# Optimization experiments

Measured on AMD Instinct MI355X. Metric: run time of the kernel, lower is better.

Reference implementation:

```python
import jax, jax.numpy as jnp
import numpy as np

D_IN = 1024
D_OUT = 1024
NUM_HEADS = 16
HEAD_DIM = D_OUT // NUM_HEADS
WINDOW = 256


def setup_inputs() -> dict:
    key = jax.random.key(0)
    ks = jax.random.split(key, 6)
    s = 0.02
    x = jax.random.normal(ks[0], (2, 2048, D_IN), dtype=jnp.float32)
    Wq = jax.random.normal(ks[1], (D_IN, D_OUT), dtype=jnp.float32) * s
    Wk = jax.random.normal(ks[2], (D_IN, D_OUT), dtype=jnp.float32) * s
    Wv = jax.random.normal(ks[3], (D_IN, D_OUT), dtype=jnp.float32) * s
    Wo = jax.random.normal(ks[4], (D_OUT, D_OUT), dtype=jnp.float32) * s
    bo = jnp.zeros((D_OUT,), dtype=jnp.float32)
    return {"x": x, "Wq": Wq, "Wk": Wk, "Wv": Wv, "Wo": Wo, "bo": bo}


def reference(x, Wq, Wk, Wv, Wo, bo):
    b, s, _ = x.shape
    # project and split heads: [b, h, s, hd]
    def heads(t):
        return t.reshape(b, s, NUM_HEADS, HEAD_DIM).transpose(0, 2, 1, 3)
    q = heads(x @ Wq)
    k = heads(x @ Wk)
    v = heads(x @ Wv)
    scores = jnp.einsum('bhqd,bhkd->bhqk', q, k) / jnp.sqrt(jnp.float32(HEAD_DIM))
    # symmetric sliding-window band: |i - j| <= WINDOW
    i = jnp.arange(s)
    band = jnp.abs(i[:, None] - i[None, :]) <= WINDOW  # [s, s]
    scores = jnp.where(band[None, None], scores, -jnp.inf)
    probs = jax.nn.softmax(scores, axis=-1)  # dropout=0.0 -> identity
    ctx = jnp.einsum('bhqk,bhkd->bhqd', probs, v)
    ctx = ctx.transpose(0, 2, 1, 3).reshape(b, s, D_OUT)
    return ctx @ Wo + bo
```

## Files before the change

### kernel.cpp

```cpp
#include <hip/hip_runtime.h>
#include <hip/hip_bf16.h>

typedef __bf16 bf16_t;
typedef __bf16 bf16x8 __attribute__((ext_vector_type(8)));
typedef __bf16 bf16x4 __attribute__((ext_vector_type(4)));
typedef float  f32x4  __attribute__((ext_vector_type(4)));

#define SEQ    2048
#define BATCH  2
#define NHEAD  16
#define HDIM   64
#define DMODEL 1024
#define WIN    256

__device__ __forceinline__ void async_load16(const void* g, void* l) {
    __builtin_amdgcn_global_load_lds(
        (const __attribute__((address_space(1))) char*)(uintptr_t)g,
        (__attribute__((address_space(3))) char*)(uintptr_t)l, 16, 0, 0);
}

__global__ __launch_bounds__(256) void prep_kernel(
    const float* __restrict__ x, const float* __restrict__ Wq,
    const float* __restrict__ Wk, const float* __restrict__ Wv,
    const float* __restrict__ Wo, bf16_t* __restrict__ xb,
    bf16_t* __restrict__ Wt) {
    const int bid = blockIdx.x, tid = threadIdx.x;
    if (bid < 1024) {
        __shared__ float t64[64][65];
        const int mat = bid >> 8, tile = bid & 255;
        const int k0 = (tile >> 4) * 64, n0 = (tile & 15) * 64;
        const float* W = (mat == 0) ? Wq : (mat == 1) ? Wk : (mat == 2) ? Wv : Wo;
        bf16_t* out = Wt + (size_t)mat * DMODEL * DMODEL;
        const int r = tid >> 4, c4 = tid & 15;
#pragma unroll
        for (int i = 0; i < 4; i++) {
            int krow = i * 16 + r;
            float4 v = *(const float4*)&W[(size_t)(k0 + krow) * DMODEL + n0 + c4 * 4];
            t64[krow][c4 * 4 + 0] = v.x; t64[krow][c4 * 4 + 1] = v.y;
            t64[krow][c4 * 4 + 2] = v.z; t64[krow][c4 * 4 + 3] = v.w;
        }
        __syncthreads();
#pragma unroll
        for (int j = 0; j < 4; j++) {
            int nrow = j * 16 + r;
            bf16x4 o;
#pragma unroll
            for (int q = 0; q < 4; q++) o[q] = (bf16_t)t64[c4 * 4 + q][nrow];
            *(bf16x4*)&out[(size_t)(n0 + nrow) * DMODEL + k0 + c4 * 4] = o;
        }
    } else {
        const int cb = bid - 1024;
#pragma unroll
        for (int it = 0; it < 4; it++) {
            int i = (cb * 4 + it) * 256 + tid;
            float4 v = ((const float4*)x)[i];
            bf16x4 o;
            o[0] = (bf16_t)v.x; o[1] = (bf16_t)v.y; o[2] = (bf16_t)v.z; o[3] = (bf16_t)v.w;
            ((bf16x4*)xb)[i] = o;
        }
    }
}

__global__ __launch_bounds__(512, 2) void gemm_qkv_kernel(
    const bf16_t* __restrict__ A, const bf16_t* __restrict__ Bt,
    bf16_t* __restrict__ Qb, bf16_t* __restrict__ Kb, bf16_t* __restrict__ Vb) {
    __shared__ __attribute__((aligned(16))) bf16_t smem[2][2][256 * 64];
    const int tid = threadIdx.x;
    const int wave = tid >> 6, lane = tid & 63, quad = lane >> 4, l15 = lane & 15;
    const int wm = wave >> 2, wn = wave & 3;
    const int id = blockIdx.x, xcd = id & 7, tt = id >> 3;
    const int gidx = xcd * 24 + tt;
    const int m0 = (gidx & 15) * 256, n0 = (gidx >> 4) * 256;

    const int cth = (tid & 7) ^ ((tid >> 3) & 7);
    const int rA = tid >> 3;

    auto stageG = [&](int tile, int gr, int buf) {
        const int row = (gr & 3) * 64 + rA;
        const bf16_t* src = (gr < 4)
            ? A  + (size_t)(m0 + row) * 1024 + tile * 64 + cth * 8
            : Bt + (size_t)(n0 + row) * 1024 + tile * 64 + cth * 8;
        async_load16(src, (char*)&smem[buf][gr >> 2][0] + (size_t)((gr & 3) * 512 + tid) * 16);
    };

    const int swz  = l15 & 7;
    const int chk0 = (quad ^ swz) * 8;
    const int chk1 = ((4 + quad) ^ swz) * 8;
    const int rowA = wm * 128 + l15;
    const int rowB = wn * 64 + l15;

    f32x4 acc[8][4] = {};

    stageG(0, 4, 0); stageG(0, 5, 0); stageG(0, 6, 0); stageG(0, 7, 0);
    stageG(0, 0, 0); stageG(0, 2, 0); stageG(0, 1, 0); stageG(0, 3, 0);
    asm volatile("s_waitcnt vmcnt(2)" ::: "memory");
    __builtin_amdgcn_s_barrier();
    __builtin_amdgcn_sched_barrier(0);

    int cur = 0;
#pragma unroll 1
    for (int t = 0; t < 16; ++t) {
        const bf16_t* as = &smem[cur][0][0];
        const bf16_t* bs = &smem[cur][1][0];
        bf16x8 am0[4], am1[4], ba0[2], ba1[2], bb0[2], bb1[2];
#pragma unroll
        for (int i = 0; i < 4; i++) {
            am0[i] = *(const bf16x8*)&as[(rowA + i * 16) * 64 + chk0];
            am1[i] = *(const bf16x8*)&as[(rowA + i * 16) * 64 + chk1];
        }
#pragma unroll
        for (int j = 0; j < 2; j++) {
            ba0[j] = *(const bf16x8*)&bs[(rowB + j * 16) * 64 + chk0];
            ba1[j] = *(const bf16x8*)&bs[(rowB + j * 16) * 64 + chk1];
        }
        if (t + 1 < 16) { stageG(t + 1, 4, cur ^ 1); stageG(t + 1, 5, cur ^ 1); }
        __builtin_amdgcn_s_barrier();
        __builtin_amdgcn_sched_barrier(0);
        __builtin_amdgcn_s_setprio(1);
#pragma unroll
        for (int i = 0; i < 4; i++)
#pragma unroll
            for (int j = 0; j < 2; j++) {
                acc[i][j] = __builtin_amdgcn_mfma_f32_16x16x32_bf16(am0[i], ba0[j], acc[i][j], 0, 0, 0);
                acc[i][j] = __builtin_amdgcn_mfma_f32_16x16x32_bf16(am1[i], ba1[j], acc[i][j], 0, 0, 0);
            }
        __builtin_amdgcn_s_setprio(0);
        __builtin_amdgcn_s_barrier();
        __builtin_amdgcn_sched_barrier(0);
#pragma unroll
        for (int j = 0; j < 2; j++) {
            bb0[j] = *(const bf16x8*)&bs[(rowB + (j + 2) * 16) * 64 + chk0];
            bb1[j] = *(const bf16x8*)&bs[(rowB + (j + 2) * 16) * 64 + chk1];
        }
        if (t + 1 < 16) { stageG(t + 1, 6, cur ^ 1); stageG(t + 1, 7, cur ^ 1); }
        __builtin_amdgcn_s_barrier();
        __builtin_amdgcn_sched_barrier(0);
        __builtin_amdgcn_s_setprio(1);
#pragma unroll
        for (int i = 0; i < 4; i++)
#pragma unroll
            for (int j = 0; j < 2; j++) {
                acc[i][j + 2] = __builtin_amdgcn_mfma_f32_16x16x32_bf16(am0[i], bb0[j], acc[i][j + 2], 0, 0, 0);
                acc[i][j + 2] = __builtin_amdgcn_mfma_f32_16x16x32_bf16(am1[i], bb1[j], acc[i][j + 2], 0, 0, 0);
            }
        __builtin_amdgcn_s_setprio(0);
        if (t + 1 < 16) asm volatile("s_waitcnt vmcnt(4)" ::: "memory");
        else            asm volatile("s_waitcnt vmcnt(0)" ::: "memory");
        __builtin_amdgcn_s_barrier();
        __builtin_amdgcn_sched_barrier(0);
#pragma unroll
        for (int i = 0; i < 4; i++) {
            am0[i] = *(const bf16x8*)&as[(rowA + (i + 4) * 16) * 64 + chk0];
            am1[i] = *(const bf16x8*)&as[(rowA + (i + 4) * 16) * 64 + chk1];
        }
        if (t + 1 < 16) { stageG(t + 1, 0, cur ^ 1); stageG(t + 1, 2, cur ^ 1); }
        __builtin_amdgcn_s_barrier();
        __builtin_amdgcn_sched_barrier(0);
        __builtin_amdgcn_s_setprio(1);
#pragma unroll
        for (int i = 0; i < 4; i++)
#pragma unroll
            for (int j = 0; j < 2; j++) {
                acc[i + 4][j + 2] = __builtin_amdgcn_mfma_f32_16x16x32_bf16(am0[i], bb0[j], acc[i + 4][j + 2], 0, 0, 0);
                acc[i + 4][j + 2] = __builtin_amdgcn_mfma_f32_16x16x32_bf16(am1[i], bb1[j], acc[i + 4][j + 2], 0, 0, 0);
            }
        __builtin_amdgcn_s_setprio(0);
        __builtin_amdgcn_s_barrier();
        __builtin_amdgcn_sched_barrier(0);
        if (t + 1 < 16) { stageG(t + 1, 1, cur ^ 1); stageG(t + 1, 3, cur ^ 1); }
        __builtin_amdgcn_s_setprio(1);
#pragma unroll
        for (int i = 0; i < 4; i++)
#pragma unroll
            for (int j = 0; j < 2; j++) {
                acc[i + 4][j] = __builtin_amdgcn_mfma_f32_16x16x32_bf16(am0[i], ba0[j], acc[i + 4][j], 0, 0, 0);
                acc[i + 4][j] = __builtin_amdgcn_mfma_f32_16x16x32_bf16(am1[i], ba1[j], acc[i + 4][j], 0, 0, 0);
            }
        __builtin_amdgcn_s_setprio(0);
        if (t + 1 < 16) {
            asm volatile("s_waitcnt vmcnt(2)" ::: "memory");
            __builtin_amdgcn_s_barrier();
            __builtin_amdgcn_sched_barrier(0);
        }
        cur ^= 1;
    }

#pragma unroll
    for (int i = 0; i < 8; i++)
#pragma unroll
        for (int j = 0; j < 4; j++)
#pragma unroll
            for (int r = 0; r < 4; r++) {
                int mg = m0 + wm * 128 + i * 16 + quad * 4 + r;
                int ng = n0 + wn * 64 + j * 16 + l15;
                float v = acc[i][j][r];
                int sel = ng >> 10, nl = ng & 1023, h = nl >> 6, d = nl & 63;
                int b = mg >> 11, s = mg & 2047;
                size_t idx = ((size_t)((b * NHEAD + h) * SEQ) + s) * HDIM + d;
                if (sel == 0)      Qb[idx] = (bf16_t)(v * 0.18033688011112042f);
                else if (sel == 1) Kb[idx] = (bf16_t)v;
                else               Vb[idx] = (bf16_t)v;
            }
}

__global__ __launch_bounds__(256) void gemm_out_kernel(
    const bf16_t* __restrict__ A, const bf16_t* __restrict__ Bt,
    float* __restrict__ Out, const float* __restrict__ bo) {
    __shared__ __attribute__((aligned(16))) bf16_t As[2][128 * 64];
    __shared__ __attribute__((aligned(16))) bf16_t Bs[2][128 * 64];
    const int tid = threadIdx.x;
    const int wave = tid >> 6, lane = tid & 63, quad = lane >> 4, l15 = lane & 15;
    const int wm = wave >> 1, wn = wave & 1;
    const int id = blockIdx.x, xcd = id & 7, t = id >> 3;
    const int m0 = t * 128, n0 = xcd * 128;

    auto stage = [&](int kt, int buf) {
#pragma unroll
        for (int i = 0; i < 4; i++) {
            int v = tid + i * 256;
            int row = v >> 3, c = (v & 7) ^ (row & 7);
            async_load16(A + (size_t)(m0 + row) * 1024 + kt * 64 + c * 8,
                         (char*)&As[buf][0] + (size_t)v * 16);
            async_load16(Bt + (size_t)(n0 + row) * 1024 + kt * 64 + c * 8,
                         (char*)&Bs[buf][0] + (size_t)v * 16);
        }
    };

    f32x4 acc[4][4] = {};
    stage(0, 0);
    __syncthreads();
    int cur = 0;
    for (int kt = 0; kt < 16; ++kt) {
        if (kt + 1 < 16) stage(kt + 1, cur ^ 1);
#pragma unroll
        for (int kk = 0; kk < 64; kk += 32) {
            bf16x8 am[4], bn[4];
#pragma unroll
            for (int i = 0; i < 4; i++) {
                int row = wm * 64 + i * 16 + l15;
                int ch = ((kk >> 3) + quad) ^ (row & 7);
                am[i] = *(const bf16x8*)&As[cur][row * 64 + ch * 8];
            }
#pragma unroll
            for (int j = 0; j < 4; j++) {
                int row = wn * 64 + j * 16 + l15;
                int ch = ((kk >> 3) + quad) ^ (row & 7);
                bn[j] = *(const bf16x8*)&Bs[cur][row * 64 + ch * 8];
            }
#pragma unroll
            for (int i = 0; i < 4; i++)
#pragma unroll
                for (int j = 0; j < 4; j++)
                    acc[i][j] = __builtin_amdgcn_mfma_f32_16x16x32_bf16(am[i], bn[j], acc[i][j], 0, 0, 0);
        }
        __syncthreads();
        cur ^= 1;
    }

#pragma unroll
    for (int i = 0; i < 4; i++)
#pragma unroll
        for (int j = 0; j < 4; j++)
#pragma unroll
            for (int r = 0; r < 4; r++) {
                int mg = m0 + wm * 64 + i * 16 + quad * 4 + r;
                int ng = n0 + wn * 64 + j * 16 + l15;
                Out[(size_t)mg * DMODEL + ng] = acc[i][j][r] + bo[ng];
            }
}

__global__ __launch_bounds__(256) void vtrans_kernel(const bf16_t* __restrict__ Vb,
                                                     bf16_t* __restrict__ Vt) {
    __shared__ bf16_t tile[64][65];
    const int bh = blockIdx.y, s0 = blockIdx.x * 64;
    const int tx = threadIdx.x, ty = threadIdx.y;
    const bf16_t* src = Vb + ((size_t)bh * SEQ + s0) * HDIM;
    bf16_t* dst = Vt + (size_t)bh * HDIM * SEQ + s0;
#pragma unroll
    for (int i = 0; i < 16; i++) {
        int row = i * 4 + ty;
        tile[row][tx] = src[(size_t)row * HDIM + tx];
    }
    __syncthreads();
#pragma unroll
    for (int i = 0; i < 16; i++) {
        int d = i * 4 + ty;
        dst[(size_t)d * SEQ + tx] = tile[tx][d];
    }
}

__global__ __launch_bounds__(512) void attn_kernel(
    const bf16_t* __restrict__ Qb, const bf16_t* __restrict__ Kb,
    const bf16_t* __restrict__ Vt, bf16_t* __restrict__ ctx) {
    __shared__ __attribute__((aligned(16))) bf16_t Ks[2][64 * 64];
    __shared__ __attribute__((aligned(16))) bf16_t Vs[2][64 * 64];
    __shared__ __attribute__((aligned(16))) bf16_t Plds[8][16][72];
    const int tid = threadIdx.x;
    const int wave = tid >> 6, lane = tid & 63, quad = lane >> 4, l15 = lane & 15;

    const int id = blockIdx.x;
    const int task = (id & 7) * 64 + (id >> 3);
    const int b = task >> 8, h = (task >> 4) & 15, Q0 = (task & 15) << 7;
    const int qbase = Q0 + wave * 16;
    const int wqt = (Q0 >> 6) + (wave >> 2);

    const bf16_t* Qp = Qb + (size_t)(b * NHEAD + h) * SEQ * HDIM;
    const bf16_t* Kp = Kb + (size_t)(b * NHEAD + h) * SEQ * HDIM;
    const bf16_t* Vp = Vt + (size_t)(b * NHEAD + h) * HDIM * SEQ;

    bf16x8 qa0 = *(const bf16x8*)(Qp + (size_t)(qbase + l15) * HDIM + quad * 8);
    bf16x8 qa1 = *(const bf16x8*)(Qp + (size_t)(qbase + l15) * HDIM + 32 + quad * 8);

    bf16x8 ones;
#pragma unroll
    for (int j = 0; j < 8; j++) ones[j] = (bf16_t)1.0f;

    f32x4 O[4] = {};
    f32x4 lacc = {};

    const int base_t = Q0 >> 6;
    const int bt0 = (base_t - 4 > 0) ? base_t - 4 : 0;
    const int bt1 = (base_t + 5 < SEQ / 64 - 1) ? base_t + 5 : SEQ / 64 - 1;

    auto stage = [&](int kt, int buf) {
        const int k0 = kt * 64;
        int v = tid;
        int row = v >> 3, c = (v & 7) ^ (row & 7);
        async_load16(Kp + (size_t)(k0 + row) * HDIM + c * 8, (char*)&Ks[buf][0] + (size_t)v * 16);
        async_load16(Vp + (size_t)row * SEQ + k0 + c * 8, (char*)&Vs[buf][0] + (size_t)v * 16);
    };

    stage(bt0, 0);
    int cb = 0;
    for (int kt = bt0; kt <= bt1; kt++) {
        __syncthreads();
        if (kt < bt1) stage(kt + 1, cb ^ 1);
        const int dt = kt - wqt;
        if (dt >= -4 && dt <= 4) {
            const int k0 = kt * 64;
            f32x4 st[4];
#pragma unroll
            for (int c = 0; c < 4; c++) {
                int row = c * 16 + l15;
                bf16x8 kb0 = *(const bf16x8*)&Ks[cb][row * 64 + (quad ^ (row & 7)) * 8];
                bf16x8 kb1 = *(const bf16x8*)&Ks[cb][row * 64 + ((quad + 4) ^ (row & 7)) * 8];
                f32x4 a = {};
                a = __builtin_amdgcn_mfma_f32_16x16x32_bf16(kb0, qa0, a, 0, 0, 0);
                a = __builtin_amdgcn_mfma_f32_16x16x32_bf16(kb1, qa1, a, 0, 0, 0);
                st[c] = a;
            }
            const bool edge = (dt == -4 || dt == 4);
            const int q = qbase + l15;
#pragma unroll
            for (int c = 0; c < 4; c++) {
                bf16x4 pk;
#pragma unroll
                for (int r = 0; r < 4; r++) {
                    float sv = st[c][r];
                    if (edge) {
                        int k = k0 + c * 16 + quad * 4 + r;
                        int dd = q - k; dd = (dd < 0) ? -dd : dd;
                        if (dd > WIN) sv = -1e30f;
                    }
                    pk[r] = (bf16_t)exp2f(sv);
                }
                *(bf16x4*)&Plds[wave][l15][c * 16 + quad * 4] = pk;
            }
            bf16x8 pa0 = *(const bf16x8*)&Plds[wave][l15][quad * 8];
            bf16x8 pa1 = *(const bf16x8*)&Plds[wave][l15][32 + quad * 8];
            lacc = __builtin_amdgcn_mfma_f32_16x16x32_bf16(pa0, ones, lacc, 0, 0, 0);
            lacc = __builtin_amdgcn_mfma_f32_16x16x32_bf16(pa1, ones, lacc, 0, 0, 0);
#pragma unroll
            for (int d = 0; d < 4; d++) {
                int row = d * 16 + l15;
                bf16x8 vb0 = *(const bf16x8*)&Vs[cb][row * 64 + (quad ^ (row & 7)) * 8];
                bf16x8 vb1 = *(const bf16x8*)&Vs[cb][row * 64 + ((quad + 4) ^ (row & 7)) * 8];
                O[d] = __builtin_amdgcn_mfma_f32_16x16x32_bf16(pa0, vb0, O[d], 0, 0, 0);
                O[d] = __builtin_amdgcn_mfma_f32_16x16x32_bf16(pa1, vb1, O[d], 0, 0, 0);
            }
        }
        cb ^= 1;
    }

#pragma unroll
    for (int r = 0; r < 4; r++) {
        float inv = 1.0f / lacc[r];
        int i = qbase + quad * 4 + r;
#pragma unroll
        for (int d = 0; d < 4; d++) {
            float v = O[d][r] * inv;
            ctx[((size_t)(b * SEQ + i)) * DMODEL + h * HDIM + d * 16 + l15] = (bf16_t)v;
        }
    }
}

extern "C" void kernel_launch(void* const* d_in, const int* in_sizes, int n_in,
                              void* d_out, int out_size, void* d_ws, size_t ws_size,
                              hipStream_t stream) {
    const float* x  = (const float*)d_in[0];
    const float* Wq = (const float*)d_in[1];
    const float* Wk = (const float*)d_in[2];
    const float* Wv = (const float*)d_in[3];
    const float* Wo = (const float*)d_in[4];
    const float* bo = (const float*)d_in[5];
    float* out = (float*)d_out;

    const size_t MTOK = (size_t)BATCH * SEQ;
    bf16_t* xb  = (bf16_t*)d_ws;
    bf16_t* Wt  = xb + MTOK * DMODEL;
    bf16_t* Qb  = Wt + (size_t)4 * DMODEL * DMODEL;
    bf16_t* Kb  = Qb + MTOK * DMODEL;
    bf16_t* Vt  = Kb + MTOK * DMODEL;
    bf16_t* ctx = Vt + MTOK * DMODEL;
    bf16_t* Vb  = ctx;

    prep_kernel<<<dim3(2048), dim3(256), 0, stream>>>(x, Wq, Wk, Wv, Wo, xb, Wt);
    gemm_qkv_kernel<<<dim3(192), dim3(512), 0, stream>>>(xb, Wt, Qb, Kb, Vb);
    vtrans_kernel<<<dim3(32, 32), dim3(64, 4), 0, stream>>>(Vb, Vt);
    attn_kernel<<<dim3(512), dim3(512), 0, stream>>>(Qb, Kb, Vt, ctx);
    gemm_out_kernel<<<dim3(256), dim3(256), 0, stream>>>(
        ctx, Wt + (size_t)3 * DMODEL * DMODEL, out, bo);
}
```

Before: 167.6 us.

## Retile QKV and output GEMMs for full CU occupancy with simpler pipeline

The QKV projection GEMM moves from 256x256 to 256x192 tiles, giving 256 blocks instead of 192 so every CU on the device gets work. Its hand-interleaved, barrier-heavy staged schedule is replaced by a plain double-buffered loop. The output GEMM halves its M tile to 64, doubling its grid to 512 blocks. The trade-off is lower per-block data reuse, and the simpler schedule gives up the fine-grained overlap of loads and MFMA work.

```diff
diff --git a/kernel.cpp b/kernel.cpp
--- a/kernel.cpp
+++ b/kernel.cpp
@@ -61,138 +61,73 @@
     }
 }
 
-__global__ __launch_bounds__(512, 2) void gemm_qkv_kernel(
+__global__ __launch_bounds__(512) void gemm_qkv_kernel(
     const bf16_t* __restrict__ A, const bf16_t* __restrict__ Bt,
     bf16_t* __restrict__ Qb, bf16_t* __restrict__ Kb, bf16_t* __restrict__ Vb) {
-    __shared__ __attribute__((aligned(16))) bf16_t smem[2][2][256 * 64];
+    __shared__ __attribute__((aligned(16))) bf16_t smem[2][(256 + 192) * 64];
     const int tid = threadIdx.x;
     const int wave = tid >> 6, lane = tid & 63, quad = lane >> 4, l15 = lane & 15;
     const int wm = wave >> 2, wn = wave & 3;
     const int id = blockIdx.x, xcd = id & 7, tt = id >> 3;
-    const int gidx = xcd * 24 + tt;
-    const int m0 = (gidx & 15) * 256, n0 = (gidx >> 4) * 256;
+    const int gidx = xcd * 32 + tt;
+    const int m0 = (gidx & 15) * 256, n0 = (gidx >> 4) * 192;
 
     const int cth = (tid & 7) ^ ((tid >> 3) & 7);
     const int rA = tid >> 3;
 
-    auto stageG = [&](int tile, int gr, int buf) {
-        const int row = (gr & 3) * 64 + rA;
-        const bf16_t* src = (gr < 4)
-            ? A  + (size_t)(m0 + row) * 1024 + tile * 64 + cth * 8
-            : Bt + (size_t)(n0 + row) * 1024 + tile * 64 + cth * 8;
-        async_load16(src, (char*)&smem[buf][gr >> 2][0] + (size_t)((gr & 3) * 512 + tid) * 16);
+    auto stage = [&](int tile, int buf) {
+#pragma unroll
+        for (int gr = 0; gr < 4; ++gr)
+            async_load16(A + (size_t)(m0 + gr * 64 + rA) * 1024 + tile * 64 + cth * 8,
+                         (char*)&smem[buf][0] + (size_t)(gr * 512 + tid) * 16);
+#pragma unroll
+        for (int gr = 0; gr < 3; ++gr)
+            async_load16(Bt + (size_t)(n0 + gr * 64 + rA) * 1024 + tile * 64 + cth * 8,
+                         (char*)&smem[buf][256 * 64] + (size_t)(gr * 512 + tid) * 16);
     };
 
     const int swz  = l15 & 7;
-    const int chk0 = (quad ^ swz) * 8;
-    const int chk1 = ((4 + quad) ^ swz) * 8;
     const int rowA = wm * 128 + l15;
-    const int rowB = wn * 64 + l15;
-
-    f32x4 acc[8][4] = {};
-
-    stageG(0, 4, 0); stageG(0, 5, 0); stageG(0, 6, 0); stageG(0, 7, 0);
-    stageG(0, 0, 0); stageG(0, 2, 0); stageG(0, 1, 0); stageG(0, 3, 0);
-    asm volatile("s_waitcnt vmcnt(2)" ::: "memory");
-    __builtin_amdgcn_s_barrier();
-    __builtin_amdgcn_sched_barrier(0);
-
+    const int rowB = wn * 48 + l15;
+
+    f32x4 acc[8][3] = {};
+
+    stage(0, 0);
+    __syncthreads();
     int cur = 0;
 #pragma unroll 1
     for (int t = 0; t < 16; ++t) {
-        const bf16_t* as = &smem[cur][0][0];
-        const bf16_t* bs = &smem[cur][1][0];
-        bf16x8 am0[4], am1[4], ba0[2], ba1[2], bb0[2], bb1[2];
-#pragma unroll
-        for (int i = 0; i < 4; i++) {
-            am0[i] = *(const bf16x8*)&as[(rowA + i * 16) * 64 + chk0];
-            am1[i] = *(const bf16x8*)&as[(rowA + i * 16) * 64 + chk1];
-        }
-#pragma unroll
-        for (int j = 0; j < 2; j++) {
-            ba0[j] = *(const bf16x8*)&bs[(rowB + j * 16) * 64 + chk0];
-            ba1[j] = *(const bf16x8*)&bs[(rowB + j * 16) * 64 + chk1];
-        }
-        if (t + 1 < 16) { stageG(t + 1, 4, cur ^ 1); stageG(t + 1, 5, cur ^ 1); }
-        __builtin_amdgcn_s_barrier();
-        __builtin_amdgcn_sched_barrier(0);
-        __builtin_amdgcn_s_setprio(1);
-#pragma unroll
-        for (int i = 0; i < 4; i++)
-#pragma unroll
-            for (int j = 0; j < 2; j++) {
-                acc[i][j] = __builtin_amdgcn_mfma_f32_16x16x32_bf16(am0[i], ba0[j], acc[i][j], 0, 0, 0);
-                acc[i][j] = __builtin_amdgcn_mfma_f32_16x16x32_bf16(am1[i], ba1[j], acc[i][j], 0, 0, 0);
-            }
-        __builtin_amdgcn_s_setprio(0);
-        __builtin_amdgcn_s_barrier();
-        __builtin_amdgcn_sched_barrier(0);
-#pragma unroll
-        for (int j = 0; j < 2; j++) {
-            bb0[j] = *(const bf16x8*)&bs[(rowB + (j + 2) * 16) * 64 + chk0];
-            bb1[j] = *(const bf16x8*)&bs[(rowB + (j + 2) * 16) * 64 + chk1];
-        }
-        if (t + 1 < 16) { stageG(t + 1, 6, cur ^ 1); stageG(t + 1, 7, cur ^ 1); }
-        __builtin_amdgcn_s_barrier();
-        __builtin_amdgcn_sched_barrier(0);
-        __builtin_amdgcn_s_setprio(1);
-#pragma unroll
-        for (int i = 0; i < 4; i++)
-#pragma unroll
-            for (int j = 0; j < 2; j++) {
-                acc[i][j + 2] = __builtin_amdgcn_mfma_f32_16x16x32_bf16(am0[i], bb0[j], acc[i][j + 2], 0, 0, 0);
-                acc[i][j + 2] = __builtin_amdgcn_mfma_f32_16x16x32_bf16(am1[i], bb1[j], acc[i][j + 2], 0, 0, 0);
-            }
-        __builtin_amdgcn_s_setprio(0);
-        if (t + 1 < 16) asm volatile("s_waitcnt vmcnt(4)" ::: "memory");
-        else            asm volatile("s_waitcnt vmcnt(0)" ::: "memory");
-        __builtin_amdgcn_s_barrier();
-        __builtin_amdgcn_sched_barrier(0);
-#pragma unroll
-        for (int i = 0; i < 4; i++) {
-            am0[i] = *(const bf16x8*)&as[(rowA + (i + 4) * 16) * 64 + chk0];
-            am1[i] = *(const bf16x8*)&as[(rowA + (i + 4) * 16) * 64 + chk1];
-        }
-        if (t + 1 < 16) { stageG(t + 1, 0, cur ^ 1); stageG(t + 1, 2, cur ^ 1); }
-        __builtin_amdgcn_s_barrier();
-        __builtin_amdgcn_sched_barrier(0);
-        __builtin_amdgcn_s_setprio(1);
-#pragma unroll
-        for (int i = 0; i < 4; i++)
-#pragma unroll
-            for (int j = 0; j < 2; j++) {
-                acc[i + 4][j + 2] = __builtin_amdgcn_mfma_f32_16x16x32_bf16(am0[i], bb0[j], acc[i + 4][j + 2], 0, 0, 0);
-                acc[i + 4][j + 2] = __builtin_amdgcn_mfma_f32_16x16x32_bf16(am1[i], bb1[j], acc[i + 4][j + 2], 0, 0, 0);
-            }
-        __builtin_amdgcn_s_setprio(0);
-        __builtin_amdgcn_s_barrier();
-        __builtin_amdgcn_sched_barrier(0);
-        if (t + 1 < 16) { stageG(t + 1, 1, cur ^ 1); stageG(t + 1, 3, cur ^ 1); }
-        __builtin_amdgcn_s_setprio(1);
-#pragma unroll
-        for (int i = 0; i < 4; i++)
-#pragma unroll
-            for (int j = 0; j < 2; j++) {
-                acc[i + 4][j] = __builtin_amdgcn_mfma_f32_16x16x32_bf16(am0[i], ba0[j], acc[i + 4][j], 0, 0, 0);
-                acc[i + 4][j] = __builtin_amdgcn_mfma_f32_16x16x32_bf16(am1[i], ba1[j], acc[i + 4][j], 0, 0, 0);
-            }
-        __builtin_amdgcn_s_setprio(0);
-        if (t + 1 < 16) {
-            asm volatile("s_waitcnt vmcnt(2)" ::: "memory");
-            __builtin_amdgcn_s_barrier();
-            __builtin_amdgcn_sched_barrier(0);
-        }
+        if (t + 1 < 16) stage(t + 1, cur ^ 1);
+        const bf16_t* as = &smem[cur][0];
+        const bf16_t* bs = &smem[cur][256 * 64];
+#pragma unroll
+        for (int kk = 0; kk < 2; ++kk) {
+            const int chk = ((kk * 4 + quad) ^ swz) * 8;
+            bf16x8 am[8], bn[3];
+#pragma unroll
+            for (int i = 0; i < 8; i++)
+                am[i] = *(const bf16x8*)&as[(rowA + i * 16) * 64 + chk];
+#pragma unroll
+            for (int j = 0; j < 3; j++)
+                bn[j] = *(const bf16x8*)&bs[(rowB + j * 16) * 64 + chk];
+#pragma unroll
+            for (int i = 0; i < 8; i++)
+#pragma unroll
+                for (int j = 0; j < 3; j++)
+                    acc[i][j] = __builtin_amdgcn_mfma_f32_16x16x32_bf16(am[i], bn[j], acc[i][j], 0, 0, 0);
+        }
+        __syncthreads();
         cur ^= 1;
     }
 
 #pragma unroll
     for (int i = 0; i < 8; i++)
 #pragma unroll
-        for (int j = 0; j < 4; j++)
+        for (int j = 0; j < 3; j++)
 #pragma unroll
             for (int r = 0; r < 4; r++) {
                 int mg = m0 + wm * 128 + i * 16 + quad * 4 + r;
-                int ng = n0 + wn * 64 + j * 16 + l15;
+                int ng = n0 + wn * 48 + j * 16 + l15;
                 float v = acc[i][j][r];
                 int sel = ng >> 10, nl = ng & 1023, h = nl >> 6, d = nl & 63;
                 int b = mg >> 11, s = mg & 2047;
@@ -206,27 +141,31 @@
 __global__ __launch_bounds__(256) void gemm_out_kernel(
     const bf16_t* __restrict__ A, const bf16_t* __restrict__ Bt,
     float* __restrict__ Out, const float* __restrict__ bo) {
-    __shared__ __attribute__((aligned(16))) bf16_t As[2][128 * 64];
+    __shared__ __attribute__((aligned(16))) bf16_t As[2][64 * 64];
     __shared__ __attribute__((aligned(16))) bf16_t Bs[2][128 * 64];
     const int tid = threadIdx.x;
-    const int wave = tid >> 6, lane = tid & 63, quad = lane >> 4, l15 = lane & 15;
-    const int wm = wave >> 1, wn = wave & 1;
-    const int id = blockIdx.x, xcd = id & 7, t = id >> 3;
-    const int m0 = t * 128, n0 = xcd * 128;
+    const int wn = tid >> 6, lane = tid & 63, quad = lane >> 4, l15 = lane & 15;
+    const int id = blockIdx.x, xcd = id & 7, mt = id >> 3;
+    const int m0 = mt * 64, n0 = xcd * 128;
 
     auto stage = [&](int kt, int buf) {
 #pragma unroll
-        for (int i = 0; i < 4; i++) {
+        for (int i = 0; i < 2; i++) {
             int v = tid + i * 256;
             int row = v >> 3, c = (v & 7) ^ (row & 7);
             async_load16(A + (size_t)(m0 + row) * 1024 + kt * 64 + c * 8,
                          (char*)&As[buf][0] + (size_t)v * 16);
+        }
+#pragma unroll
+        for (int i = 0; i < 4; i++) {
+            int v = tid + i * 256;
+            int row = v >> 3, c = (v & 7) ^ (row & 7);
             async_load16(Bt + (size_t)(n0 + row) * 1024 + kt * 64 + c * 8,
                          (char*)&Bs[buf][0] + (size_t)v * 16);
         }
     };
 
-    f32x4 acc[4][4] = {};
+    f32x4 acc[4][2] = {};
     stage(0, 0);
     __syncthreads();
     int cur = 0;
@@ -234,23 +173,23 @@
         if (kt + 1 < 16) stage(kt + 1, cur ^ 1);
 #pragma unroll
         for (int kk = 0; kk < 64; kk += 32) {
-            bf16x8 am[4], bn[4];
+            bf16x8 am[4], bn[2];
 #pragma unroll
             for (int i = 0; i < 4; i++) {
-                int row = wm * 64 + i * 16 + l15;
+                int row = i * 16 + l15;
                 int ch = ((kk >> 3) + quad) ^ (row & 7);
                 am[i] = *(const bf16x8*)&As[cur][row * 64 + ch * 8];
             }
 #pragma unroll
-            for (int j = 0; j < 4; j++) {
-                int row = wn * 64 + j * 16 + l15;
+            for (int j = 0; j < 2; j++) {
+                int row = wn * 32 + j * 16 + l15;
                 int ch = ((kk >> 3) + quad) ^ (row & 7);
                 bn[j] = *(const bf16x8*)&Bs[cur][row * 64 + ch * 8];
             }
 #pragma unroll
             for (int i = 0; i < 4; i++)
 #pragma unroll
-                for (int j = 0; j < 4; j++)
+                for (int j = 0; j < 2; j++)
                     acc[i][j] = __builtin_amdgcn_mfma_f32_16x16x32_bf16(am[i], bn[j], acc[i][j], 0, 0, 0);
         }
         __syncthreads();
@@ -260,11 +199,11 @@
 #pragma unroll
     for (int i = 0; i < 4; i++)
 #pragma unroll
-        for (int j = 0; j < 4; j++)
+        for (int j = 0; j < 2; j++)
 #pragma unroll
             for (int r = 0; r < 4; r++) {
-                int mg = m0 + wm * 64 + i * 16 + quad * 4 + r;
-                int ng = n0 + wn * 64 + j * 16 + l15;
+                int mg = m0 + i * 16 + quad * 4 + r;
+                int ng = n0 + wn * 32 + j * 16 + l15;
                 Out[(size_t)mg * DMODEL + ng] = acc[i][j][r] + bo[ng];
             }
 }
@@ -415,9 +354,9 @@
     bf16_t* Vb  = ctx;
 
     prep_kernel<<<dim3(2048), dim3(256), 0, stream>>>(x, Wq, Wk, Wv, Wo, xb, Wt);
-    gemm_qkv_kernel<<<dim3(192), dim3(512), 0, stream>>>(xb, Wt, Qb, Kb, Vb);
+    gemm_qkv_kernel<<<dim3(256), dim3(512), 0, stream>>>(xb, Wt, Qb, Kb, Vb);
     vtrans_kernel<<<dim3(32, 32), dim3(64, 4), 0, stream>>>(Vb, Vt);
     attn_kernel<<<dim3(512), dim3(512), 0, stream>>>(Qb, Kb, Vt, ctx);
-    gemm_out_kernel<<<dim3(256), dim3(256), 0, stream>>>(
+    gemm_out_kernel<<<dim3(512), dim3(256), 0, stream>>>(
         ctx, Wt + (size_t)3 * DMODEL * DMODEL, out, bo);
 }
```

Measured after the change: 159.4 us. -4.9%, faster.
